# Kernel tuning notes

Hardware: AMD Instinct MI355X
Metric: run time of the kernel (lower is better)

Reference implementation:

```python
import jax, jax.numpy as jnp
import numpy as np

N = 128          # cube side (voxels)
LPIX = 3.0       # Mpc per voxel (hardcoded in dsq_loss.forward)
KBINS = 100      # radial k bins (hardcoded)
LOSS_WEIGHT = 1.0


def _binning(n, lpix, kbins):
    # Static radial k-bin assignment computed once with numpy.
    kf = 2.0 * np.pi * np.fft.fftfreq(n, d=lpix)
    kx, ky, kz = np.meshgrid(kf, kf, kf, indexing='ij')
    kmag = np.sqrt(kx * kx + ky * ky + kz * kz).ravel()  # [n^3]
    pos = kmag > 0
    edges = np.linspace(kmag[pos].min(), kmag.max(), kbins + 1)
    ids = np.clip(np.digitize(kmag, edges) - 1, 0, kbins - 1)
    ids = np.where(pos, ids, kbins)  # route k=0 (DC) mode to a dropped bin
    counts = np.bincount(ids[pos], minlength=kbins).astype(np.float32)
    kcent = 0.5 * (edges[:-1] + edges[1:])
    return ids.astype(np.int32), counts, kcent.astype(np.float32)

_IDS, _COUNTS, _KCENT = _binning(N, LPIX, KBINS)


def _dsq(x):
    # x: [B, 1, N, N, N] -> dimensionless power spectrum Delta^2(k): [B, KBINS]
    b = x.shape[0]
    fk = jnp.fft.fftn(x, axes=(-3, -2, -1))
    # P(k) estimator: |delta_k|^2 * Lpix^3 / N^3  (Lpix^6/V with V=(N*Lpix)^3)
    pk = (fk.real ** 2 + fk.imag ** 2) * (LPIX ** 3 / float(N ** 3))
    pk = pk.reshape(b, -1).T  # [N^3, B]
    sums = jax.ops.segment_sum(pk, jnp.asarray(_IDS), num_segments=KBINS + 1)[:KBINS]
    cnt = jnp.asarray(_COUNTS)[:, None]
    pmean = jnp.where(cnt > 0, sums / jnp.maximum(cnt, 1.0), jnp.nan)  # [KBINS, B]
    kc = jnp.asarray(_KCENT)[:, None]
    dsq = pmean * kc ** 3 / (2.0 * jnp.pi ** 2)
    return dsq.T  # [B, KBINS]


def setup_inputs() -> dict:
    key = jax.random.key(0)
    k1, k2 = jax.random.split(key)
    # positive brightness-temperature-like fields so log10(Delta^2) is finite
    pred = jax.random.uniform(k1, (8, 1, N, N, N), dtype=jnp.float32) + 0.1
    target = jax.random.uniform(k2, (8, 1, N, N, N), dtype=jnp.float32) + 0.1
    return {"pred": pred, "target": target}


def reference(pred, target):
    dsq_hr = _dsq(target)
    dsq_sr = _dsq(pred)
    loss = jnp.nanmean(jnp.abs(jnp.log10(dsq_hr) - jnp.log10(dsq_sr)))
    return LOSS_WEIGHT * loss
```

## Files before the change

### kernel.cpp

```cpp
#include <hip/hip_runtime.h>
#include <math.h>

#ifndef M_PI
#define M_PI 3.14159265358979323846
#endif

#define NSIDE 128
#define NVOX  2097152
#define KBINS 100
#define NFIELDS 16
#define NORMF (27.0f / 2097152.0f)
#define FSTRIDE ((size_t)65 * 16384)

#define WS_SUMS_OFF   0
#define WS_CNT_OFF    6464
#define WS_OCT_OFF    8192
#define WS_TRANS_OFF  282880

__device__ __forceinline__ double bin_edge(int i, double start, double step, double stop) {
    if (i == 100) return stop;
    return __dadd_rn(__dmul_rn((double)i, step), start);
}

__device__ __forceinline__ void bin_params(double* start, double* step, double* stop) {
    const double inv   = 1.0 / 384.0;
    const double twopi = 2.0 * M_PI;
    double k1 = __dmul_rn(twopi, __dmul_rn(1.0, inv));
    *start = sqrt(__dadd_rn(__dadd_rn(0.0, 0.0), __dmul_rn(k1, k1)));
    double k64 = __dmul_rn(twopi, __dmul_rn(-64.0, inv));
    double s64 = __dmul_rn(k64, k64);
    *stop = sqrt(__dadd_rn(__dadd_rn(s64, s64), s64));
    *step = (*stop - *start) / 100.0;
}

__device__ int compute_bin(int ix, int iy, int iz) {
    const double inv   = 1.0 / 384.0;
    const double twopi = 2.0 * M_PI;
    double fx = (double)(ix < 64 ? ix : ix - 128);
    double fy = (double)(iy < 64 ? iy : iy - 128);
    double fz = (double)(iz < 64 ? iz : iz - 128);
    double kx = __dmul_rn(twopi, __dmul_rn(fx, inv));
    double ky = __dmul_rn(twopi, __dmul_rn(fy, inv));
    double kz = __dmul_rn(twopi, __dmul_rn(fz, inv));
    double sq = __dadd_rn(__dadd_rn(__dmul_rn(kx, kx), __dmul_rn(ky, ky)), __dmul_rn(kz, kz));
    double kmag = sqrt(sq);
    if (!(kmag > 0.0)) return 100;
    double start, step, stop;
    bin_params(&start, &step, &stop);
    double t = (kmag - start) / step;
    int c = (int)floor(t);
    if (c < -1) c = -1;
    if (c > 100) c = 100;
    while (c < 100 && kmag >= bin_edge(c + 1, start, step, stop)) ++c;
    while (c >= 0 && kmag < bin_edge(c, start, step, stop)) --c;
    if (c < 0) c = 0;
    if (c > 99) c = 99;
    return c;
}


__device__ __forceinline__ int br5(int v) { return (int)(__brev((unsigned)v) >> 27); }

__device__ __forceinline__ float2 cmul(float2 a, float2 w) {
    return make_float2(a.x * w.x - a.y * w.y, a.x * w.y + a.y * w.x);
}
__device__ __forceinline__ float2 twid(float r) {
    return make_float2(__builtin_amdgcn_cosf(r), __builtin_amdgcn_sinf(r));
}

__device__ __forceinline__ void fft128_regs(float2 r[4], int l) {
    {
        float2 a0 = r[0], a1 = r[1], a2 = r[2], a3 = r[3];
        float2 s0 = make_float2(a0.x + a2.x, a0.y + a2.y);
        float2 d0 = make_float2(a0.x - a2.x, a0.y - a2.y);
        float2 s1 = make_float2(a1.x + a3.x, a1.y + a3.y);
        float2 d1 = make_float2(a1.x - a3.x, a1.y - a3.y);
        float2 b0 = make_float2(s0.x + s1.x, s0.y + s1.y);
        float2 b2 = make_float2(s0.x - s1.x, s0.y - s1.y);
        float2 b1 = make_float2(d0.x + d1.y, d0.y - d1.x);
        float2 b3 = make_float2(d0.x - d1.y, d0.y + d1.x);
        float base = -(float)l * (1.0f / 128.0f);
        float2 w1 = twid(base), w2 = twid(2.0f * base), w3 = twid(3.0f * base);
        r[0] = b0;
        r[1] = cmul(b1, w1);
        r[2] = cmul(b2, w2);
        r[3] = cmul(b3, w3);
    }
#pragma unroll
    for (int h = 16; h >= 1; h >>= 1) {
        bool hi = (l & h) != 0;
        float2 W = twid(-(float)(l & (h - 1)) / (float)(2 * h));
#pragma unroll
        for (int j = 0; j < 4; ++j) {
            float2 x = r[j];
            float2 v = make_float2(__shfl_xor(x.x, h, 64), __shfl_xor(x.y, h, 64));
            float2 sum = make_float2(x.x + v.x, x.y + v.y);
            float2 dif = make_float2(v.x - x.x, v.y - x.y);
            float2 tw  = cmul(dif, W);
            r[j] = hi ? tw : sum;
        }
    }
}

__global__ __launch_bounds__(256) void k_zero(float* sums, int* counts) {
    int t = blockIdx.x * 256 + threadIdx.x;
    if (t < NFIELDS * 101) sums[t] = 0.0f;
    if (t < 101) counts[t] = 0;
}

__global__ __launch_bounds__(256) void k_oct(unsigned char* __restrict__ oct,
                                             int* __restrict__ counts) {
    __shared__ int lcnt[4][104];
    int tid = threadIdx.x;
#pragma unroll
    for (int j = tid; j < 4 * 104; j += 256) ((int*)lcnt)[j] = 0;
    __syncthreads();
    int idx = blockIdx.x * 256 + tid;
    if (idx < 65 * 65 * 65) {
        int c = idx % 65;
        int r = idx / 65;
        int b = r % 65;
        int a = r / 65;
        int id = compute_bin(a, b, c);
        oct[c * 4225 + a * 65 + b] = (unsigned char)id;
        if (id < 100) {
            int w = ((a == 0 || a == 64) ? 1 : 2) *
                    ((b == 0 || b == 64) ? 1 : 2) *
                    ((c == 0 || c == 64) ? 1 : 2);
            atomicAdd(&lcnt[tid & 3][id], w);
        }
    }
    __syncthreads();
    if (tid < 101) {
        int tot = lcnt[0][tid] + lcnt[1][tid] + lcnt[2][tid] + lcnt[3][tid];
        if (tot) atomicAdd(&counts[tid], tot);
    }
}

__global__ __launch_bounds__(1024, 8) void k_fft_z(const float* __restrict__ pred,
                                                   const float* __restrict__ target,
                                                   float2* __restrict__ A) {
    __shared__ float2 L[32][129];
    int t = threadIdx.x;
    int l = t & 31;
    int row = t >> 5;
    int x  = blockIdx.x >> 2;
    int y0 = (blockIdx.x & 3) << 5;
    int f = blockIdx.y;
    const float* in = (f < 8) ? (pred + (size_t)f * NVOX)
                              : (target + (size_t)(f - 8) * NVOX);
    const float* src = in + (size_t)x * 16384 + (size_t)(y0 + row) * 128;
    float2 r[4];
#pragma unroll
    for (int j = 0; j < 4; ++j) r[j] = make_float2(src[l + 32 * j], 0.0f);
    fft128_regs(r, l);
#pragma unroll
    for (int j = 0; j < 4; ++j) L[row][l + 32 * j] = r[j];
    __syncthreads();
    float2* dst = A + (size_t)f * FSTRIDE;
#pragma unroll
    for (int i = 0; i < 3; ++i) {
        int kk = (t >> 5) + 32 * i;
        int dy = t & 31;
        if (kk <= 64) {
            int slot = br5(kk >> 2) + 32 * (kk & 3);
            dst[(size_t)kk * 16384 + (size_t)x * 128 + y0 + dy] = L[dy][slot];
        }
    }
}

__global__ __launch_bounds__(1024, 8) void k_fft_y(float2* __restrict__ A) {
    int t = threadIdx.x;
    int l = t & 31;
    int row = t >> 5;
    int kz = blockIdx.x >> 2;
    int xg = blockIdx.x & 3;
    int f = blockIdx.y;
    float2* base = A + (size_t)f * FSTRIDE + (size_t)kz * 16384
                     + (size_t)(xg * 32 + row) * 128;
    float2 r[4];
#pragma unroll
    for (int j = 0; j < 4; ++j) r[j] = base[l + 32 * j];
    fft128_regs(r, l);
#pragma unroll
    for (int j = 0; j < 4; ++j) base[l + 32 * j] = r[j];
}

__global__ __launch_bounds__(1024, 8) void k_fft_x_bin(const float2* __restrict__ A,
                                                       const unsigned char* __restrict__ oct,
                                                       float* __restrict__ sums) {
    __shared__ float2 L[32][129];
    __shared__ float lbins[8][104];
    __shared__ unsigned char ltab[4225];
    int t = threadIdx.x;
    int kz = blockIdx.x >> 2;
    int s0 = (blockIdx.x & 3) << 5;
    int f = blockIdx.y;
    const float2* base = A + (size_t)f * FSTRIDE + (size_t)kz * 16384;
    for (int j = t; j < 8 * 104; j += 1024) ((float*)lbins)[j] = 0.0f;
    for (int j = t; j < 4225; j += 1024) ltab[j] = oct[kz * 4225 + j];
#pragma unroll
    for (int i = 0; i < 2; ++i) {
        int n = t + 1024 * i;
        int x = n >> 4;
        int m = n & 15;
        float4 v = *(const float4*)(base + (size_t)x * 128 + s0 + 2 * m);
        L[2 * m][x]     = make_float2(v.x, v.y);
        L[2 * m + 1][x] = make_float2(v.z, v.w);
    }
    __syncthreads();
    int l = t & 31;
    int yc = t >> 5;
    float2 r[4];
#pragma unroll
    for (int j = 0; j < 4; ++j) r[j] = L[yc][l + 32 * j];
    fft128_regs(r, l);
    int p = s0 + yc;
    int ky = 4 * br5(p & 31) + (p >> 5);
    int mky = (ky <= 64) ? ky : 128 - ky;
#pragma unroll
    for (int j = 0; j < 4; ++j) {
        int kx = 4 * br5(l) + j;
        int mkx = (kx <= 64) ? kx : 128 - kx;
        float2 c = r[j];
        float pk = c.x * c.x + c.y * c.y;
        atomicAdd(&lbins[t & 7][ltab[mkx * 65 + mky]], pk);
    }
    __syncthreads();
    if (t < 101) {
        float wz = (kz == 0 || kz == 64) ? 1.0f : 2.0f;
        float v = lbins[0][t] + lbins[1][t] + lbins[2][t] + lbins[3][t] +
                  lbins[4][t] + lbins[5][t] + lbins[6][t] + lbins[7][t];
        if (v != 0.0f) atomicAdd(&sums[f * 101 + t], v * (NORMF) * wz);
    }
}

__global__ __launch_bounds__(128) void k_finalize(const float* __restrict__ sums,
                                                  const int* __restrict__ counts,
                                                  float* __restrict__ out) {
    __shared__ double ssum[128];
    __shared__ int scnt[128];
    int k = threadIdx.x;
    double local = 0.0;
    int nloc = 0;
    if (k < KBINS) {
        int c = counts[k];
        if (c > 0) {
            double start, step, stop;
            bin_params(&start, &step, &stop);
            double e0 = bin_edge(k, start, step, stop);
            double e1 = bin_edge(k + 1, start, step, stop);
            float kc  = (float)(0.5 * (e0 + e1));
            float kc3 = kc * kc * kc;
            const float two_pi2 = (float)(2.0 * M_PI * M_PI);
            float cf = (float)c;
            for (int b = 0; b < 8; ++b) {
                float pm_p = sums[b * 101 + k] / cf;
                float pm_t = sums[(8 + b) * 101 + k] / cf;
                float dsq_p = pm_p * kc3 / two_pi2;
                float dsq_t = pm_t * kc3 / two_pi2;
                float d = fabsf(log10f(dsq_t) - log10f(dsq_p));
                local += (double)d;
            }
            nloc = 8;
        }
    }
    ssum[k] = local;
    scnt[k] = nloc;
    __syncthreads();
    for (int off = 64; off > 0; off >>= 1) {
        if (k < off) { ssum[k] += ssum[k + off]; scnt[k] += scnt[k + off]; }
        __syncthreads();
    }
    if (k == 0) out[0] = (float)(ssum[0] / (double)scnt[0]);
}

extern "C" void kernel_launch(void* const* d_in, const int* in_sizes, int n_in,
                              void* d_out, int out_size, void* d_ws, size_t ws_size,
                              hipStream_t stream) {
    (void)in_sizes; (void)n_in; (void)out_size; (void)ws_size;
    const float* pred   = (const float*)d_in[0];
    const float* target = (const float*)d_in[1];
    float* out = (float*)d_out;
    char* ws = (char*)d_ws;

    float* sums        = (float*)(ws + WS_SUMS_OFF);
    int* counts        = (int*)(ws + WS_CNT_OFF);
    unsigned char* oct = (unsigned char*)(ws + WS_OCT_OFF);
    float2* A          = (float2*)(ws + WS_TRANS_OFF);

    k_zero<<<7, 256, 0, stream>>>(sums, counts);
    k_oct<<<(65 * 65 * 65 + 255) / 256, 256, 0, stream>>>(oct, counts);

    k_fft_z<<<dim3(512, NFIELDS), 1024, 0, stream>>>(pred, target, A);
    k_fft_y<<<dim3(65 * 4, NFIELDS), 1024, 0, stream>>>(A);
    k_fft_x_bin<<<dim3(65 * 4, NFIELDS), 1024, 0, stream>>>(A, oct, sums);

    k_finalize<<<1, 128, 0, stream>>>(sums, counts, out);
}
```

Measured before the change: 360.6 us.

## Switch 128-point FFT to 8 lanes x 16 registers per line, drop LDS transposes

The 128-point FFT is restructured so each line uses 8 lanes holding 16 elements each. Four radix-2 stages run in registers and only three use cross-lane shuffles, instead of 32 lanes with four elements and five shuffle stages. The z-pass now writes bit-reversed outputs directly to global memory, and the x-pass reads strided columns directly, removing both shared-memory transposes and their barriers. Block size drops from 1024 to 256 threads. The trade-off is higher register pressure and less coalesced global access (strided z writes and x reads).

After: 342.3 us. 5.1% less time.

```diff
diff --git a/kernel.cpp b/kernel.cpp
--- a/kernel.cpp
+++ b/kernel.cpp
@@ -59,8 +59,13 @@
 }
 
 
-__device__ __forceinline__ int br5(int v) { return (int)(__brev((unsigned)v) >> 27); }
-
+__device__ __forceinline__ int br3(int v) { return ((v & 1) << 2) | (v & 2) | ((v >> 2) & 1); }
+__device__ __forceinline__ int br4(int v) {
+    return ((v & 1) << 3) | ((v & 2) << 1) | ((v & 4) >> 1) | ((v & 8) >> 3);
+}
+
+__device__ __forceinline__ float2 f2add(float2 a, float2 b) { return make_float2(a.x + b.x, a.y + b.y); }
+__device__ __forceinline__ float2 f2sub(float2 a, float2 b) { return make_float2(a.x - b.x, a.y - b.y); }
 __device__ __forceinline__ float2 cmul(float2 a, float2 w) {
     return make_float2(a.x * w.x - a.y * w.y, a.x * w.y + a.y * w.x);
 }
@@ -68,36 +73,64 @@
     return make_float2(__builtin_amdgcn_cosf(r), __builtin_amdgcn_sinf(r));
 }
 
-__device__ __forceinline__ void fft128_regs(float2 r[4], int l) {
+__device__ __forceinline__ void fft128_r16(float2 r[16], int m) {
+    const float fm = (float)m;
+#pragma unroll
+    for (int j = 0; j < 8; ++j) {
+        float2 W = twid(-(fm + 8.0f * (float)j) * (1.0f / 128.0f));
+        float2 a = r[j], b = r[j + 8];
+        r[j]     = f2add(a, b);
+        r[j + 8] = cmul(f2sub(a, b), W);
+    }
+#pragma unroll
+    for (int j = 0; j < 4; ++j) {
+        float2 W = twid(-(fm + 8.0f * (float)j) * (1.0f / 64.0f));
+#pragma unroll
+        for (int half = 0; half < 16; half += 8) {
+            float2 a = r[half + j], b = r[half + j + 4];
+            r[half + j]     = f2add(a, b);
+            r[half + j + 4] = cmul(f2sub(a, b), W);
+        }
+    }
+#pragma unroll
+    for (int j = 0; j < 2; ++j) {
+        float2 W = twid(-(fm + 8.0f * (float)j) * (1.0f / 32.0f));
+#pragma unroll
+        for (int q = 0; q < 16; q += 4) {
+            float2 a = r[q + j], b = r[q + j + 2];
+            r[q + j]     = f2add(a, b);
+            r[q + j + 2] = cmul(f2sub(a, b), W);
+        }
+    }
     {
-        float2 a0 = r[0], a1 = r[1], a2 = r[2], a3 = r[3];
-        float2 s0 = make_float2(a0.x + a2.x, a0.y + a2.y);
-        float2 d0 = make_float2(a0.x - a2.x, a0.y - a2.y);
-        float2 s1 = make_float2(a1.x + a3.x, a1.y + a3.y);
-        float2 d1 = make_float2(a1.x - a3.x, a1.y - a3.y);
-        float2 b0 = make_float2(s0.x + s1.x, s0.y + s1.y);
-        float2 b2 = make_float2(s0.x - s1.x, s0.y - s1.y);
-        float2 b1 = make_float2(d0.x + d1.y, d0.y - d1.x);
-        float2 b3 = make_float2(d0.x - d1.y, d0.y + d1.x);
-        float base = -(float)l * (1.0f / 128.0f);
-        float2 w1 = twid(base), w2 = twid(2.0f * base), w3 = twid(3.0f * base);
-        r[0] = b0;
-        r[1] = cmul(b1, w1);
-        r[2] = cmul(b2, w2);
-        r[3] = cmul(b3, w3);
-    }
-#pragma unroll
-    for (int h = 16; h >= 1; h >>= 1) {
-        bool hi = (l & h) != 0;
-        float2 W = twid(-(float)(l & (h - 1)) / (float)(2 * h));
-#pragma unroll
-        for (int j = 0; j < 4; ++j) {
+        float2 W = twid(-fm * (1.0f / 16.0f));
+#pragma unroll
+        for (int q = 0; q < 16; q += 2) {
+            float2 a = r[q], b = r[q + 1];
+            r[q]     = f2add(a, b);
+            r[q + 1] = cmul(f2sub(a, b), W);
+        }
+    }
+#pragma unroll
+    for (int h = 4; h >= 2; h >>= 1) {
+        bool hi = (m & h) != 0;
+        float2 W = twid(-(float)(m & (h - 1)) / (float)(2 * h));
+#pragma unroll
+        for (int j = 0; j < 16; ++j) {
             float2 x = r[j];
             float2 v = make_float2(__shfl_xor(x.x, h, 64), __shfl_xor(x.y, h, 64));
-            float2 sum = make_float2(x.x + v.x, x.y + v.y);
-            float2 dif = make_float2(v.x - x.x, v.y - x.y);
-            float2 tw  = cmul(dif, W);
-            r[j] = hi ? tw : sum;
+            float2 s = f2add(x, v);
+            float2 d = cmul(f2sub(v, x), W);
+            r[j] = hi ? d : s;
+        }
+    }
+    {
+        bool hi = (m & 1) != 0;
+#pragma unroll
+        for (int j = 0; j < 16; ++j) {
+            float2 x = r[j];
+            float2 v = make_float2(__shfl_xor(x.x, 1, 64), __shfl_xor(x.y, 1, 64));
+            r[j] = hi ? f2sub(v, x) : f2add(x, v);
         }
     }
 }
@@ -137,93 +170,77 @@
     }
 }
 
-__global__ __launch_bounds__(1024, 8) void k_fft_z(const float* __restrict__ pred,
-                                                   const float* __restrict__ target,
-                                                   float2* __restrict__ A) {
-    __shared__ float2 L[32][129];
+__global__ __launch_bounds__(256, 6) void k_fft_z(const float* __restrict__ pred,
+                                                  const float* __restrict__ target,
+                                                  float2* __restrict__ A) {
     int t = threadIdx.x;
-    int l = t & 31;
-    int row = t >> 5;
+    int m = t & 7, row = t >> 3;
     int x  = blockIdx.x >> 2;
     int y0 = (blockIdx.x & 3) << 5;
     int f = blockIdx.y;
     const float* in = (f < 8) ? (pred + (size_t)f * NVOX)
                               : (target + (size_t)(f - 8) * NVOX);
     const float* src = in + (size_t)x * 16384 + (size_t)(y0 + row) * 128;
-    float2 r[4];
-#pragma unroll
-    for (int j = 0; j < 4; ++j) r[j] = make_float2(src[l + 32 * j], 0.0f);
-    fft128_regs(r, l);
-#pragma unroll
-    for (int j = 0; j < 4; ++j) L[row][l + 32 * j] = r[j];
-    __syncthreads();
-    float2* dst = A + (size_t)f * FSTRIDE;
-#pragma unroll
-    for (int i = 0; i < 3; ++i) {
-        int kk = (t >> 5) + 32 * i;
-        int dy = t & 31;
-        if (kk <= 64) {
-            int slot = br5(kk >> 2) + 32 * (kk & 3);
-            dst[(size_t)kk * 16384 + (size_t)x * 128 + y0 + dy] = L[dy][slot];
-        }
-    }
-}
-
-__global__ __launch_bounds__(1024, 8) void k_fft_y(float2* __restrict__ A) {
+    float2 r[16];
+#pragma unroll
+    for (int j = 0; j < 16; ++j) r[j] = make_float2(src[m + 8 * j], 0.0f);
+    fft128_r16(r, m);
+    float2* dst = A + (size_t)f * FSTRIDE + (size_t)x * 128 + (y0 + row);
+    int b3 = br3(m);
+    if (b3 < 4) {
+#pragma unroll
+        for (int j = 0; j < 16; ++j) {
+            int kz = 16 * b3 + br4(j);
+            dst[(size_t)kz * 16384] = r[j];
+        }
+    } else if (b3 == 4) {
+        dst[(size_t)64 * 16384] = r[0];
+    }
+}
+
+__global__ __launch_bounds__(256, 6) void k_fft_y(float2* __restrict__ A) {
     int t = threadIdx.x;
-    int l = t & 31;
-    int row = t >> 5;
+    int m = t & 7, g = t >> 3;
     int kz = blockIdx.x >> 2;
     int xg = blockIdx.x & 3;
     int f = blockIdx.y;
     float2* base = A + (size_t)f * FSTRIDE + (size_t)kz * 16384
-                     + (size_t)(xg * 32 + row) * 128;
-    float2 r[4];
-#pragma unroll
-    for (int j = 0; j < 4; ++j) r[j] = base[l + 32 * j];
-    fft128_regs(r, l);
-#pragma unroll
-    for (int j = 0; j < 4; ++j) base[l + 32 * j] = r[j];
-}
-
-__global__ __launch_bounds__(1024, 8) void k_fft_x_bin(const float2* __restrict__ A,
-                                                       const unsigned char* __restrict__ oct,
-                                                       float* __restrict__ sums) {
-    __shared__ float2 L[32][129];
+                     + (size_t)(xg * 32 + g) * 128;
+    float2 r[16];
+#pragma unroll
+    for (int j = 0; j < 16; ++j) r[j] = base[m + 8 * j];
+    fft128_r16(r, m);
+#pragma unroll
+    for (int j = 0; j < 16; ++j) base[m + 8 * j] = r[j];
+}
+
+__global__ __launch_bounds__(256, 6) void k_fft_x_bin(const float2* __restrict__ A,
+                                                      const unsigned char* __restrict__ oct,
+                                                      float* __restrict__ sums) {
     __shared__ float lbins[8][104];
     __shared__ unsigned char ltab[4225];
     int t = threadIdx.x;
+    int m = t & 7, g = t >> 3;
     int kz = blockIdx.x >> 2;
     int s0 = (blockIdx.x & 3) << 5;
     int f = blockIdx.y;
-    const float2* base = A + (size_t)f * FSTRIDE + (size_t)kz * 16384;
-    for (int j = t; j < 8 * 104; j += 1024) ((float*)lbins)[j] = 0.0f;
-    for (int j = t; j < 4225; j += 1024) ltab[j] = oct[kz * 4225 + j];
-#pragma unroll
-    for (int i = 0; i < 2; ++i) {
-        int n = t + 1024 * i;
-        int x = n >> 4;
-        int m = n & 15;
-        float4 v = *(const float4*)(base + (size_t)x * 128 + s0 + 2 * m);
-        L[2 * m][x]     = make_float2(v.x, v.y);
-        L[2 * m + 1][x] = make_float2(v.z, v.w);
-    }
-    __syncthreads();
-    int l = t & 31;
-    int yc = t >> 5;
-    float2 r[4];
-#pragma unroll
-    for (int j = 0; j < 4; ++j) r[j] = L[yc][l + 32 * j];
-    fft128_regs(r, l);
-    int p = s0 + yc;
-    int ky = 4 * br5(p & 31) + (p >> 5);
+    for (int j = t; j < 8 * 104; j += 256) ((float*)lbins)[j] = 0.0f;
+    for (int j = t; j < 4225; j += 256) ltab[j] = oct[kz * 4225 + j];
+    const float2* base = A + (size_t)f * FSTRIDE + (size_t)kz * 16384 + (s0 + g);
+    float2 r[16];
+#pragma unroll
+    for (int j = 0; j < 16; ++j) r[j] = base[(size_t)(m + 8 * j) * 128];
+    fft128_r16(r, m);
+    __syncthreads();
+    int p = s0 + g;
+    int ky = (br3(p & 7) << 4) | br4(p >> 3);
     int mky = (ky <= 64) ? ky : 128 - ky;
-#pragma unroll
-    for (int j = 0; j < 4; ++j) {
-        int kx = 4 * br5(l) + j;
+    int b3x = br3(m) << 4;
+#pragma unroll
+    for (int j = 0; j < 16; ++j) {
+        int kx = b3x | br4(j);
         int mkx = (kx <= 64) ? kx : 128 - kx;
-        float2 c = r[j];
-        float pk = c.x * c.x + c.y * c.y;
+        float pk = r[j].x * r[j].x + r[j].y * r[j].y;
         atomicAdd(&lbins[t & 7][ltab[mkx * 65 + mky]], pk);
     }
     __syncthreads();
@@ -292,9 +309,9 @@
     k_zero<<<7, 256, 0, stream>>>(sums, counts);
     k_oct<<<(65 * 65 * 65 + 255) / 256, 256, 0, stream>>>(oct, counts);
 
-    k_fft_z<<<dim3(512, NFIELDS), 1024, 0, stream>>>(pred, target, A);
-    k_fft_y<<<dim3(65 * 4, NFIELDS), 1024, 0, stream>>>(A);
-    k_fft_x_bin<<<dim3(65 * 4, NFIELDS), 1024, 0, stream>>>(A, oct, sums);
+    k_fft_z<<<dim3(512, NFIELDS), 256, 0, stream>>>(pred, target, A);
+    k_fft_y<<<dim3(65 * 4, NFIELDS), 256, 0, stream>>>(A);
+    k_fft_x_bin<<<dim3(65 * 4, NFIELDS), 256, 0, stream>>>(A, oct, sums);
 
     k_finalize<<<1, 128, 0, stream>>>(sums, counts, out);
 }
```
